# Performance work log

Hardware: AMD Instinct MI355X
Metric: run time of the kernel (lower is better)

Reference implementation:

```python
import jax, jax.numpy as jnp
import numpy as np

# 8-bit signed quantizer bounds and integer-rescale constant (from module attrs)
X1_LO, X1_HI = -128.0, 127.0
X2_LO, X2_HI = -128.0, 127.0
Y_LO, Y_HI = -128.0, 127.0
G_VALUE = 16.0


def setup_inputs() -> dict:
    key = jax.random.key(0)
    k1, k2 = jax.random.split(key)
    # Pre-quantized integer activations stored as float32 (as in int-infer mode)
    x1 = jnp.round(jnp.clip(jax.random.normal(k1, (2, 16, 2048, 64), dtype=jnp.float32) * 40.0, X1_LO, X1_HI))
    x2 = jnp.round(jnp.clip(jax.random.normal(k2, (2, 16, 64, 2048), dtype=jnp.float32) * 40.0, X2_LO, X2_HI))
    return {
        "x1": x1,
        "x2": x2,
        "scale1_last_layer": jnp.float32(0.1),
        "scale_x1": jnp.float32(0.05),
        "scale2_last_layer": jnp.float32(0.08),
        "scale_x2": jnp.float32(0.04),
    }


def _div_shift(x, scale_prev, scale_cur, lo, hi):
    # round(x * s_prev / s_cur) then clamp to quantizer bounds
    return jnp.clip(jnp.round(x * (scale_prev / scale_cur)), lo, hi)


def reference(x1, x2, scale1_last_layer, scale_x1, scale2_last_layer, scale_x2):
    # _forward_infer: rescale both operands, integer matmul, /G, round, clip
    x1_int = _div_shift(x1, scale1_last_layer, scale_x1, X1_LO, X1_HI)
    x2_int = _div_shift(x2, scale2_last_layer, scale_x2, X2_LO, X2_HI)
    # [b, h, s, d] @ [b, h, d, s] -> [b, h, s, s]
    y_int = jnp.clip(jnp.round(jnp.matmul(x1_int, x2_int) / G_VALUE), Y_LO, Y_HI)
    return y_int
```

## Files before the change

### kernel.cpp

```cpp
#include <hip/hip_runtime.h>


typedef int   v4i  __attribute__((ext_vector_type(4)));
typedef int   v16i __attribute__((ext_vector_type(16)));
typedef float v4f  __attribute__((ext_vector_type(4)));

static constexpr int BATCH = 32;
static constexpr int SEQ   = 2048;
static constexpr int DIM   = 64;
static constexpr int TILE  = 128;
static constexpr int TPB   = 256;
static constexpr int TPS   = SEQ / TILE;
static constexpr int TPBATCH = TPS * TPS;
static constexpr int NBLK  = BATCH * TPBATCH;

__global__ __launch_bounds__(TPB) void oint_mm_kernel(
    const float* __restrict__ x1,
    const float* __restrict__ x2,
    const float* __restrict__ p_s1ll,
    const float* __restrict__ p_sx1,
    const float* __restrict__ p_s2ll,
    const float* __restrict__ p_sx2,
    float* __restrict__ out)
{
    __shared__ float slab[64 * 128];

    const float r1 = p_s1ll[0] / p_sx1[0];
    const float r2 = p_s2ll[0] / p_sx2[0];

    const int bid     = (int)blockIdx.x;
    const int logical = (bid & 7) * (NBLK >> 3) + (bid >> 3);

    const int batch = logical >> 8;
    const int t     = logical & (TPBATCH - 1);
    const int tm    = t >> 4;
    const int tn    = t & (TPS - 1);

    const float* Abase = x1 + (size_t)batch * SEQ * DIM;
    const float* Bbase = x2 + (size_t)batch * DIM * SEQ;
    float*       Obase = out + (size_t)batch * SEQ * SEQ;

    const int tid  = (int)threadIdx.x;
    const int lane = tid & 63;
    const int wave = tid >> 6;
    const int wr   = wave >> 1;
    const int wc   = wave & 1;

    const int mbase = tm * TILE + wr * 64;
    const int nbase = tn * TILE + wc * 64;

    const int lc = lane & 31;
    const int kh = lane >> 5;

    v4i bfrag[2][2];
    #pragma unroll
    for (int fn = 0; fn < 2; ++fn) {
        #pragma unroll
        for (int s = 0; s < 2; ++s) {
            const float* src = Bbase + (size_t)(s * 32 + kh * 16) * SEQ + (nbase + fn * 32 + lc);
            v4i pk;
            #pragma unroll
            for (int d = 0; d < 4; ++d) {
                int dw = 0;
                #pragma unroll
                for (int j = 0; j < 4; ++j) {
                    float q = rintf(src[(size_t)(4 * d + j) * SEQ] * r2);
                    q = fminf(fmaxf(q, -128.f), 127.f);
                    dw |= ((int)q & 0xFF) << (8 * j);
                }
                pk[d] = dw;
            }
            bfrag[fn][s] = pk;
        }
    }

    #pragma unroll
    for (int fm = 0; fm < 2; ++fm) {
        if (fm) __syncthreads();

        v4i af[2];
        #pragma unroll
        for (int s = 0; s < 2; ++s) {
            const float* src = Abase + (size_t)(mbase + fm * 32 + lc) * DIM + s * 32 + kh * 16;
            v4i pk;
            #pragma unroll
            for (int d = 0; d < 4; ++d) {
                v4f v = *(const v4f*)(src + 4 * d);
                int dw = 0;
                #pragma unroll
                for (int j = 0; j < 4; ++j) {
                    float q = rintf(v[j] * r1);
                    q = fminf(fmaxf(q, -128.f), 127.f);
                    dw |= ((int)q & 0xFF) << (8 * j);
                }
                pk[d] = dw;
            }
            af[s] = pk;
        }

        #pragma unroll
        for (int fn = 0; fn < 2; ++fn) {
            v16i z = {0,0,0,0,0,0,0,0,0,0,0,0,0,0,0,0};
            v16i acc = __builtin_amdgcn_mfma_i32_32x32x32_i8(af[0], bfrag[fn][0], z,   0, 0, 0);
            acc      = __builtin_amdgcn_mfma_i32_32x32x32_i8(af[1], bfrag[fn][1], acc, 0, 0, 0);

            #pragma unroll
            for (int r = 0; r < 16; ++r) {
                const int rloc = (r & 3) + 8 * (r >> 2) + 4 * kh;
                const int sr   = wr * 32 + rloc;
                const int c    = wc * 64 + fn * 32 + lc;
                float v = rintf((float)acc[r] * 0.0625f);
                v = fminf(fmaxf(v, -128.f), 127.f);
                slab[sr * 128 + c] = v;
            }
        }

        __syncthreads();

        #pragma unroll
        for (int i = 0; i < 8; ++i) {
            const int f  = i * TPB + tid;
            const int sr = f >> 5;
            const int cq = f & 31;
            v4f v = *(const v4f*)&slab[sr * 128 + cq * 4];
            const int grow = tm * TILE + ((sr >> 5) << 6) + fm * 32 + (sr & 31);
            __builtin_nontemporal_store(
                v, (v4f*)(Obase + (size_t)grow * SEQ + tn * TILE + cq * 4));
        }
    }
}

extern "C" void kernel_launch(void* const* d_in, const int* in_sizes, int n_in,
                              void* d_out, int out_size, void* d_ws, size_t ws_size,
                              hipStream_t stream) {
    (void)in_sizes; (void)n_in; (void)out_size; (void)d_ws; (void)ws_size;
    oint_mm_kernel<<<NBLK, TPB, 0, stream>>>(
        (const float*)d_in[0], (const float*)d_in[1],
        (const float*)d_in[2], (const float*)d_in[3],
        (const float*)d_in[4], (const float*)d_in[5],
        (float*)d_out);
}
```

Before: 106.1 us.

## Prepack quantized int8 operands in a separate kernel before the MFMA matmul

Adds a prepass kernel that rescales, rounds, clamps and packs both inputs into int8 MFMA fragment layout in workspace, then the matmul kernel loads packed fragments directly. This removes repeated float loads and quantization work that each output tile did redundantly. It adds an extra launch and a workspace round trip, and falls back to the fused kernel if workspace is too small.

Result: faster. 100.4 us (-5.3%).

```diff
diff --git a/kernel.cpp b/kernel.cpp
--- a/kernel.cpp
+++ b/kernel.cpp
@@ -13,20 +13,66 @@
 static constexpr int TPS   = SEQ / TILE;
 static constexpr int TPBATCH = TPS * TPS;
 static constexpr int NBLK  = BATCH * TPBATCH;
-
-__global__ __launch_bounds__(TPB) void oint_mm_kernel(
-    const float* __restrict__ x1,
-    const float* __restrict__ x2,
-    const float* __restrict__ p_s1ll,
-    const float* __restrict__ p_sx1,
-    const float* __restrict__ p_s2ll,
-    const float* __restrict__ p_sx2,
+static constexpr size_t PKB = (size_t)BATCH * SEQ * DIM;
+
+__device__ __forceinline__ int qpack4(v4f v, float r) {
+    int dw = 0;
+    #pragma unroll
+    for (int j = 0; j < 4; ++j) {
+        float q = rintf(v[j] * r);
+        q = fminf(fmaxf(q, -128.f), 127.f);
+        dw |= ((int)q & 0xFF) << (8 * j);
+    }
+    return dw;
+}
+
+__global__ __launch_bounds__(256) void prepack_kernel(
+    const float* __restrict__ x1, const float* __restrict__ x2,
+    const float* __restrict__ p_s1ll, const float* __restrict__ p_sx1,
+    const float* __restrict__ p_s2ll, const float* __restrict__ p_sx2,
+    char* __restrict__ A8, char* __restrict__ B8)
+{
+    const int bid = (int)blockIdx.x;
+    const int tid = (int)threadIdx.x;
+    if (bid < 1024) {
+        const float r1 = p_s1ll[0] / p_sx1[0];
+        const int t  = bid * 256 + tid;
+        const int b  = t >> 13;
+        const int m  = (t >> 2) & 2047;
+        const int kq = t & 3;
+        const float* src = x1 + (size_t)t * 16;
+        v4i pk;
+        #pragma unroll
+        for (int d = 0; d < 4; ++d) pk[d] = qpack4(*(const v4f*)(src + 4 * d), r1);
+        *(v4i*)(A8 + ((size_t)(b * 4 + kq) * SEQ + m) * 16) = pk;
+    } else {
+        const float r2 = p_s2ll[0] / p_sx2[0];
+        const int t  = (bid - 1024) * 256 + tid;
+        const int b  = t >> 13;
+        const int kq = (t >> 11) & 3;
+        const int n  = t & 2047;
+        const float* src = x2 + (size_t)b * DIM * SEQ + (size_t)(kq * 16) * SEQ + n;
+        v4i pk;
+        #pragma unroll
+        for (int d = 0; d < 4; ++d) {
+            int dw = 0;
+            #pragma unroll
+            for (int j = 0; j < 4; ++j) {
+                float q = rintf(src[(size_t)(4 * d + j) * SEQ] * r2);
+                q = fminf(fmaxf(q, -128.f), 127.f);
+                dw |= ((int)q & 0xFF) << (8 * j);
+            }
+            pk[d] = dw;
+        }
+        *(v4i*)(B8 + (size_t)t * 16) = pk;
+    }
+}
+
+__global__ __launch_bounds__(TPB) void oint_mm_packed(
+    const char* __restrict__ A8, const char* __restrict__ B8,
     float* __restrict__ out)
 {
     __shared__ float slab[64 * 128];
-
-    const float r1 = p_s1ll[0] / p_sx1[0];
-    const float r2 = p_s2ll[0] / p_sx2[0];
 
     const int bid     = (int)blockIdx.x;
     const int logical = (bid & 7) * (NBLK >> 3) + (bid >> 3);
@@ -36,9 +82,7 @@
     const int tm    = t >> 4;
     const int tn    = t & (TPS - 1);
 
-    const float* Abase = x1 + (size_t)batch * SEQ * DIM;
-    const float* Bbase = x2 + (size_t)batch * DIM * SEQ;
-    float*       Obase = out + (size_t)batch * SEQ * SEQ;
+    float* Obase = out + (size_t)batch * SEQ * SEQ;
 
     const int tid  = (int)threadIdx.x;
     const int lane = tid & 63;
@@ -49,6 +93,84 @@
     const int mbase = tm * TILE + wr * 64;
     const int nbase = tn * TILE + wc * 64;
 
+    const int lc = lane & 31;
+    const int kh = lane >> 5;
+
+    v4i bfrag[2][2];
+    #pragma unroll
+    for (int fn = 0; fn < 2; ++fn)
+        #pragma unroll
+        for (int s = 0; s < 2; ++s)
+            bfrag[fn][s] = *(const v4i*)(
+                B8 + ((size_t)(batch * 4 + s * 2 + kh) * SEQ + nbase + fn * 32 + lc) * 16);
+
+    #pragma unroll
+    for (int fm = 0; fm < 2; ++fm) {
+        if (fm) __syncthreads();
+
+        v4i af[2];
+        #pragma unroll
+        for (int s = 0; s < 2; ++s)
+            af[s] = *(const v4i*)(
+                A8 + ((size_t)(batch * 4 + s * 2 + kh) * SEQ + mbase + fm * 32 + lc) * 16);
+
+        #pragma unroll
+        for (int fn = 0; fn < 2; ++fn) {
+            v16i z = {0,0,0,0,0,0,0,0,0,0,0,0,0,0,0,0};
+            v16i acc = __builtin_amdgcn_mfma_i32_32x32x32_i8(af[0], bfrag[fn][0], z,   0, 0, 0);
+            acc      = __builtin_amdgcn_mfma_i32_32x32x32_i8(af[1], bfrag[fn][1], acc, 0, 0, 0);
+
+            #pragma unroll
+            for (int r = 0; r < 16; ++r) {
+                const int rloc = (r & 3) + 8 * (r >> 2) + 4 * kh;
+                const int sr   = wr * 32 + rloc;
+                const int c    = wc * 64 + fn * 32 + lc;
+                float v = rintf((float)acc[r] * 0.0625f);
+                v = fminf(fmaxf(v, -128.f), 127.f);
+                slab[sr * 128 + c] = v;
+            }
+        }
+
+        __syncthreads();
+
+        #pragma unroll
+        for (int i = 0; i < 8; ++i) {
+            const int f  = i * TPB + tid;
+            const int sr = f >> 5;
+            const int cq = f & 31;
+            v4f v = *(const v4f*)&slab[sr * 128 + cq * 4];
+            const int grow = tm * TILE + ((sr >> 5) << 6) + fm * 32 + (sr & 31);
+            __builtin_nontemporal_store(
+                v, (v4f*)(Obase + (size_t)grow * SEQ + tn * TILE + cq * 4));
+        }
+    }
+}
+
+__global__ __launch_bounds__(TPB) void oint_mm_fused(
+    const float* __restrict__ x1, const float* __restrict__ x2,
+    const float* __restrict__ p_s1ll, const float* __restrict__ p_sx1,
+    const float* __restrict__ p_s2ll, const float* __restrict__ p_sx2,
+    float* __restrict__ out)
+{
+    __shared__ float slab[64 * 128];
+    const float r1 = p_s1ll[0] / p_sx1[0];
+    const float r2 = p_s2ll[0] / p_sx2[0];
+    const int bid     = (int)blockIdx.x;
+    const int logical = (bid & 7) * (NBLK >> 3) + (bid >> 3);
+    const int batch = logical >> 8;
+    const int t     = logical & (TPBATCH - 1);
+    const int tm    = t >> 4;
+    const int tn    = t & (TPS - 1);
+    const float* Abase = x1 + (size_t)batch * SEQ * DIM;
+    const float* Bbase = x2 + (size_t)batch * DIM * SEQ;
+    float*       Obase = out + (size_t)batch * SEQ * SEQ;
+    const int tid  = (int)threadIdx.x;
+    const int lane = tid & 63;
+    const int wave = tid >> 6;
+    const int wr   = wave >> 1;
+    const int wc   = wave & 1;
+    const int mbase = tm * TILE + wr * 64;
+    const int nbase = tn * TILE + wc * 64;
     const int lc = lane & 31;
     const int kh = lane >> 5;
 
@@ -73,37 +195,23 @@
             bfrag[fn][s] = pk;
         }
     }
-
     #pragma unroll
     for (int fm = 0; fm < 2; ++fm) {
         if (fm) __syncthreads();
-
         v4i af[2];
         #pragma unroll
         for (int s = 0; s < 2; ++s) {
             const float* src = Abase + (size_t)(mbase + fm * 32 + lc) * DIM + s * 32 + kh * 16;
             v4i pk;
             #pragma unroll
-            for (int d = 0; d < 4; ++d) {
-                v4f v = *(const v4f*)(src + 4 * d);
-                int dw = 0;
-                #pragma unroll
-                for (int j = 0; j < 4; ++j) {
-                    float q = rintf(v[j] * r1);
-                    q = fminf(fmaxf(q, -128.f), 127.f);
-                    dw |= ((int)q & 0xFF) << (8 * j);
-                }
-                pk[d] = dw;
-            }
+            for (int d = 0; d < 4; ++d) pk[d] = qpack4(*(const v4f*)(src + 4 * d), r1);
             af[s] = pk;
         }
-
         #pragma unroll
         for (int fn = 0; fn < 2; ++fn) {
             v16i z = {0,0,0,0,0,0,0,0,0,0,0,0,0,0,0,0};
             v16i acc = __builtin_amdgcn_mfma_i32_32x32x32_i8(af[0], bfrag[fn][0], z,   0, 0, 0);
             acc      = __builtin_amdgcn_mfma_i32_32x32x32_i8(af[1], bfrag[fn][1], acc, 0, 0, 0);
-
             #pragma unroll
             for (int r = 0; r < 16; ++r) {
                 const int rloc = (r & 3) + 8 * (r >> 2) + 4 * kh;
@@ -114,9 +222,7 @@
                 slab[sr * 128 + c] = v;
             }
         }
-
         __syncthreads();
-
         #pragma unroll
         for (int i = 0; i < 8; ++i) {
             const int f  = i * TPB + tid;
@@ -133,10 +239,21 @@
 extern "C" void kernel_launch(void* const* d_in, const int* in_sizes, int n_in,
                               void* d_out, int out_size, void* d_ws, size_t ws_size,
                               hipStream_t stream) {
-    (void)in_sizes; (void)n_in; (void)out_size; (void)d_ws; (void)ws_size;
-    oint_mm_kernel<<<NBLK, TPB, 0, stream>>>(
-        (const float*)d_in[0], (const float*)d_in[1],
-        (const float*)d_in[2], (const float*)d_in[3],
-        (const float*)d_in[4], (const float*)d_in[5],
-        (float*)d_out);
-}
+    (void)in_sizes; (void)n_in; (void)out_size;
+    const float* x1 = (const float*)d_in[0];
+    const float* x2 = (const float*)d_in[1];
+    const float* s1 = (const float*)d_in[2];
+    const float* s2 = (const float*)d_in[3];
+    const float* s3 = (const float*)d_in[4];
+    const float* s4 = (const float*)d_in[5];
+    float* out = (float*)d_out;
+
+    if (ws_size >= 2 * PKB) {
+        char* A8 = (char*)d_ws;
+        char* B8 = (char*)d_ws + PKB;
+        prepack_kernel<<<2048, 256, 0, stream>>>(x1, x2, s1, s2, s3, s4, A8, B8);
+        oint_mm_packed<<<NBLK, TPB, 0, stream>>>(A8, B8, out);
+    } else {
+        oint_mm_fused<<<NBLK, TPB, 0, stream>>>(x1, x2, s1, s2, s3, s4, out);
+    }
+}
```

## Prepack quantized int8 operands in a separate kernel before the MFMA matmul

Applied to the files above, without the earlier changes.

Adds a prepass kernel that quantizes x1 and x2 once into int8 buffers in workspace, laid out in the MFMA fragment order. The matmul kernel then loads the ready-made fragments instead of re-quantizing float inputs in every tile. Output stores also switch from nontemporal to regular stores. This removes redundant quantization and strided float reads, at the cost of an extra kernel launch and a workspace round trip. The output write traffic, which dominates, is unchanged.

Result: no change. 107.8 us (+1.6%).

```diff
diff --git a/kernel.cpp b/kernel.cpp
--- a/kernel.cpp
+++ b/kernel.cpp
@@ -13,20 +13,66 @@
 static constexpr int TPS   = SEQ / TILE;
 static constexpr int TPBATCH = TPS * TPS;
 static constexpr int NBLK  = BATCH * TPBATCH;
+static constexpr size_t PKB = (size_t)BATCH * SEQ * DIM;
 
-__global__ __launch_bounds__(TPB) void oint_mm_kernel(
-    const float* __restrict__ x1,
-    const float* __restrict__ x2,
-    const float* __restrict__ p_s1ll,
-    const float* __restrict__ p_sx1,
-    const float* __restrict__ p_s2ll,
-    const float* __restrict__ p_sx2,
+__device__ __forceinline__ int qpack4(v4f v, float r) {
+    int dw = 0;
+    #pragma unroll
+    for (int j = 0; j < 4; ++j) {
+        float q = rintf(v[j] * r);
+        q = fminf(fmaxf(q, -128.f), 127.f);
+        dw |= ((int)q & 0xFF) << (8 * j);
+    }
+    return dw;
+}
+
+__global__ __launch_bounds__(256) void prepack_kernel(
+    const float* __restrict__ x1, const float* __restrict__ x2,
+    const float* __restrict__ p_s1ll, const float* __restrict__ p_sx1,
+    const float* __restrict__ p_s2ll, const float* __restrict__ p_sx2,
+    char* __restrict__ A8, char* __restrict__ B8)
+{
+    const int bid = (int)blockIdx.x;
+    const int tid = (int)threadIdx.x;
+    if (bid < 1024) {
+        const float r1 = p_s1ll[0] / p_sx1[0];
+        const int t  = bid * 256 + tid;
+        const int b  = t >> 13;
+        const int m  = (t >> 2) & 2047;
+        const int kq = t & 3;
+        const float* src = x1 + (size_t)t * 16;
+        v4i pk;
+        #pragma unroll
+        for (int d = 0; d < 4; ++d) pk[d] = qpack4(*(const v4f*)(src + 4 * d), r1);
+        *(v4i*)(A8 + ((size_t)(b * 4 + kq) * SEQ + m) * 16) = pk;
+    } else {
+        const float r2 = p_s2ll[0] / p_sx2[0];
+        const int t  = (bid - 1024) * 256 + tid;
+        const int b  = t >> 13;
+        const int kq = (t >> 11) & 3;
+        const int n  = t & 2047;
+        const float* src = x2 + (size_t)b * DIM * SEQ + (size_t)(kq * 16) * SEQ + n;
+        v4i pk;
+        #pragma unroll
+        for (int d = 0; d < 4; ++d) {
+            int dw = 0;
+            #pragma unroll
+            for (int j = 0; j < 4; ++j) {
+                float q = rintf(src[(size_t)(4 * d + j) * SEQ] * r2);
+                q = fminf(fmaxf(q, -128.f), 127.f);
+                dw |= ((int)q & 0xFF) << (8 * j);
+            }
+            pk[d] = dw;
+        }
+        *(v4i*)(B8 + (size_t)t * 16) = pk;
+    }
+}
+
+__global__ __launch_bounds__(TPB) void oint_mm_packed(
+    const char* __restrict__ A8, const char* __restrict__ B8,
     float* __restrict__ out)
 {
     __shared__ float slab[64 * 128];
-
-    const float r1 = p_s1ll[0] / p_sx1[0];
-    const float r2 = p_s2ll[0] / p_sx2[0];
 
     const int bid     = (int)blockIdx.x;
     const int logical = (bid & 7) * (NBLK >> 3) + (bid >> 3);
@@ -36,9 +82,7 @@
     const int tm    = t >> 4;
     const int tn    = t & (TPS - 1);
 
-    const float* Abase = x1 + (size_t)batch * SEQ * DIM;
-    const float* Bbase = x2 + (size_t)batch * DIM * SEQ;
-    float*       Obase = out + (size_t)batch * SEQ * SEQ;
+    float* Obase = out + (size_t)batch * SEQ * SEQ;
 
     const int tid  = (int)threadIdx.x;
     const int lane = tid & 63;
@@ -54,25 +98,11 @@
 
     v4i bfrag[2][2];
     #pragma unroll
-    for (int fn = 0; fn < 2; ++fn) {
+    for (int fn = 0; fn < 2; ++fn)
         #pragma unroll
-        for (int s = 0; s < 2; ++s) {
-            const float* src = Bbase + (size_t)(s * 32 + kh * 16) * SEQ + (nbase + fn * 32 + lc);
-            v4i pk;
-            #pragma unroll
-            for (int d = 0; d < 4; ++d) {
-                int dw = 0;
-                #pragma unroll
-                for (int j = 0; j < 4; ++j) {
-                    float q = rintf(src[(size_t)(4 * d + j) * SEQ] * r2);
-                    q = fminf(fmaxf(q, -128.f), 127.f);
-                    dw |= ((int)q & 0xFF) << (8 * j);
-                }
-                pk[d] = dw;
-            }
-            bfrag[fn][s] = pk;
-        }
-    }
+        for (int s = 0; s < 2; ++s)
+            bfrag[fn][s] = *(const v4i*)(
+                B8 + ((size_t)(batch * 4 + s * 2 + kh) * SEQ + nbase + fn * 32 + lc) * 16);
 
     #pragma unroll
     for (int fm = 0; fm < 2; ++fm) {
@@ -80,23 +110,9 @@
 
         v4i af[2];
         #pragma unroll
-        for (int s = 0; s < 2; ++s) {
-            const float* src = Abase + (size_t)(mbase + fm * 32 + lc) * DIM + s * 32 + kh * 16;
-            v4i pk;
-            #pragma unroll
-            for (int d = 0; d < 4; ++d) {
-                v4f v = *(const v4f*)(src + 4 * d);
-                int dw = 0;
-                #pragma unroll
-                for (int j = 0; j < 4; ++j) {
-                    float q = rintf(v[j] * r1);
-                    q = fminf(fmaxf(q, -128.f), 127.f);
-                    dw |= ((int)q & 0xFF) << (8 * j);
-                }
-                pk[d] = dw;
-            }
-            af[s] = pk;
-        }
+        for (int s = 0; s < 2; ++s)
+            af[s] = *(const v4i*)(
+                A8 + ((size_t)(batch * 4 + s * 2 + kh) * SEQ + mbase + fm * 32 + lc) * 16);
 
         #pragma unroll
         for (int fn = 0; fn < 2; ++fn) {
@@ -124,8 +140,7 @@
             const int cq = f & 31;
             v4f v = *(const v4f*)&slab[sr * 128 + cq * 4];
             const int grow = tm * TILE + ((sr >> 5) << 6) + fm * 32 + (sr & 31);
-            __builtin_nontemporal_store(
-                v, (v4f*)(Obase + (size_t)grow * SEQ + tn * TILE + cq * 4));
+            *(v4f*)(Obase + (size_t)grow * SEQ + tn * TILE + cq * 4) = v;
         }
     }
 }
@@ -133,10 +148,17 @@
 extern "C" void kernel_launch(void* const* d_in, const int* in_sizes, int n_in,
                               void* d_out, int out_size, void* d_ws, size_t ws_size,
                               hipStream_t stream) {
-    (void)in_sizes; (void)n_in; (void)out_size; (void)d_ws; (void)ws_size;
-    oint_mm_kernel<<<NBLK, TPB, 0, stream>>>(
-        (const float*)d_in[0], (const float*)d_in[1],
-        (const float*)d_in[2], (const float*)d_in[3],
-        (const float*)d_in[4], (const float*)d_in[5],
-        (float*)d_out);
+    (void)in_sizes; (void)n_in; (void)out_size;
+    const float* x1 = (const float*)d_in[0];
+    const float* x2 = (const float*)d_in[1];
+    const float* s1 = (const float*)d_in[2];
+    const float* s2 = (const float*)d_in[3];
+    const float* s3 = (const float*)d_in[4];
+    const float* s4 = (const float*)d_in[5];
+    float* out = (float*)d_out;
+
+    char* A8 = (char*)d_ws;
+    char* B8 = (char*)d_ws + PKB;
+    prepack_kernel<<<2048, 256, 0, stream>>>(x1, x2, s1, s2, s3, s4, A8, B8);
+    oint_mm_packed<<<NBLK, TPB, 0, stream>>>(A8, B8, out);
 }
```
